# Kernel optimization log

Measured on AMD Instinct MI355X. Metric: run time of the kernel, lower is better.

The kernel has to match this reference:

```python
import jax, jax.numpy as jnp
import numpy as np

N_NODES = 100000
N_EDGES = 1000000
D_IN = 128
D_H = 128
N_CLS = 16


def setup_inputs() -> dict:
    key = jax.random.key(0)
    ks = jax.random.split(key, 12)
    s_in = 1.0 / np.sqrt(D_IN)
    s_h = 1.0 / np.sqrt(D_H)
    s_2h = 1.0 / np.sqrt(2 * D_H)
    return {
        "x": jax.random.normal(ks[0], (N_NODES, D_IN), jnp.float32),
        "edge_index": jax.random.randint(ks[1], (2, N_EDGES), 0, N_NODES, jnp.int64),
        "W_l0": jax.random.normal(ks[2], (D_H, D_IN), jnp.float32) * s_in,
        "b_l0": jnp.zeros((D_H,), jnp.float32),
        "W_r0": jax.random.normal(ks[3], (D_H, D_IN), jnp.float32) * s_in,
        "W_l1": jax.random.normal(ks[4], (D_H, D_H), jnp.float32) * s_h,
        "b_l1": jnp.zeros((D_H,), jnp.float32),
        "W_r1": jax.random.normal(ks[5], (D_H, D_H), jnp.float32) * s_h,
        "W_c": jax.random.normal(ks[6], (D_H, 2 * D_H), jnp.float32) * s_2h,
        "b_c": jnp.zeros((D_H,), jnp.float32),
        "W_o": jax.random.normal(ks[7], (N_CLS, 2 * D_H), jnp.float32) * s_2h,
        "b_o": jnp.zeros((N_CLS,), jnp.float32),
    }


def _sage_conv(x, src, dst, W_l, b_l, W_r, num_nodes):
    # PyG SAGEConv (mean aggr): lin_l(mean of source-neighbor feats) + lin_r(x)
    msgs = x[src]  # [E, d] gather
    agg = jax.ops.segment_sum(msgs, dst, num_segments=num_nodes)
    cnt = jax.ops.segment_sum(jnp.ones((src.shape[0],), x.dtype), dst, num_segments=num_nodes)
    mean = agg / jnp.maximum(cnt, 1.0)[:, None]
    return mean @ W_l.T + b_l + x @ W_r.T


def reference(x, edge_index, W_l0, b_l0, W_r0, W_l1, b_l1, W_r1, W_c, b_c, W_o, b_o):
    src, dst = edge_index[0], edge_index[1]
    n = x.shape[0]
    for W_l, b_l, W_r in ((W_l0, b_l0, W_r0), (W_l1, b_l1, W_r1)):
        x_old = x
        h = jax.nn.relu(_sage_conv(x, src, dst, W_l, b_l, W_r, n))
        x = jnp.concatenate([x_old, h], axis=-1)  # [N, 2*hidden]
        x = jax.nn.relu(x @ W_c.T + b_c)
        # dropout: identity (eval mode)
    edge_feats = jnp.concatenate([x[src], x[dst]], axis=-1)  # [E, 2*hidden]
    return edge_feats @ W_o.T + b_o
```

## Files before the change

kernel.cpp:

```cpp
#include <hip/hip_runtime.h>
#include <hip/hip_bf16.h>

#define NN 100000
#define NE 1000000
#define D  128
#define NC 16

typedef short short8 __attribute__((ext_vector_type(8)));
typedef float f32x4  __attribute__((ext_vector_type(4)));

__device__ __forceinline__ float bf2f(ushort u) {
  union { unsigned int i; float f; } v; v.i = ((unsigned int)u) << 16; return v.f;
}
__device__ __forceinline__ ushort f2bf(float f) {
  union { float f; unsigned int i; } v; v.f = f;
  unsigned int x = v.i;
  return (ushort)((x + 0x7FFFu + ((x >> 16) & 1u)) >> 16);
}

__global__ void sniff_k(const ushort* __restrict__ xr, const unsigned int* __restrict__ ei,
                        int* __restrict__ flags) {
  if (threadIdx.x != 0 || blockIdx.x != 0) return;
  int f32 = 0;
  for (int i = 0; i < 128; ++i) {
    unsigned int e = ((unsigned int)xr[i] >> 7) & 0xFFu;
    if (e < 97u || e > 157u) f32 = 1;
  }
  flags[0] = f32;
  unsigned int s = 0;
  for (int i = 1; i < 256; i += 2) s |= ei[i];
  flags[1] = (s == 0) ? 1 : 0;
}

__global__ void convert_idx_k(const int* __restrict__ ei, const int* __restrict__ flags,
                              int* __restrict__ idx, int n) {
  int i = blockIdx.x * blockDim.x + threadIdx.x;
  if (i >= n) return;
  int v = flags[1] ? ei[2 * i] : ei[i];
  v = v < 0 ? 0 : (v >= NN ? NN - 1 : v);
  idx[i] = v;
}

__global__ void convert_x_k(const void* __restrict__ xin, const int* __restrict__ flags,
                            ushort* __restrict__ xb) {
  int i = blockIdx.x * blockDim.x + threadIdx.x;
  const int n4 = NN * D / 4;
  if (i >= n4) return;
  ushort4 o;
  if (flags[0]) {
    float4 v = ((const float4*)xin)[i];
    o.x = f2bf(v.x); o.y = f2bf(v.y); o.z = f2bf(v.z); o.w = f2bf(v.w);
  } else {
    o = ((const ushort4*)xin)[i];
  }
  ((ushort4*)xb)[i] = o;
}

struct WPtrs { const void* p[10]; };
#define WTOT 102800
__global__ void convert_w_k(WPtrs w, const int* __restrict__ flags, ushort* __restrict__ wb) {
  const int off[10] = {0, 16384, 32768, 49152, 65536, 98304, 102400, 102528, 102656, 102784};
  int i = blockIdx.x * blockDim.x + threadIdx.x;
  if (i >= WTOT) return;
  int seg = 0;
  #pragma unroll
  for (int s2 = 1; s2 < 10; ++s2) if (i >= off[s2]) seg = s2;
  int j = i - off[seg];
  wb[i] = flags[0] ? f2bf(((const float*)w.p[seg])[j]) : ((const ushort*)w.p[seg])[j];
}

#define BSH 9
#define NBKT ((NN + 511) >> BSH)
#define MS_NBLK 256
#define MS_EPB ((NE + MS_NBLK - 1) / MS_NBLK)
#define CSR_CAP 8192

__global__ __launch_bounds__(256) void hist_k(const int* __restrict__ dst,
                                              int* __restrict__ bhist) {
  __shared__ int h[NBKT];
  for (int t = threadIdx.x; t < NBKT; t += 256) h[t] = 0;
  __syncthreads();
  const int stride = gridDim.x * blockDim.x;
  for (int i = blockIdx.x * blockDim.x + threadIdx.x; i < NE; i += stride)
    atomicAdd(&h[dst[i] >> BSH], 1);
  __syncthreads();
  for (int t = threadIdx.x; t < NBKT; t += 256) if (h[t]) atomicAdd(&bhist[t], h[t]);
}

__global__ __launch_bounds__(256) void scanb_k(const int* __restrict__ bhist,
                                               int* __restrict__ bstart,
                                               int* __restrict__ bcur) {
  __shared__ int tmp[256];
  const int t = threadIdx.x;
  int v = (t < NBKT) ? bhist[t] : 0;
  tmp[t] = v;
  __syncthreads();
  for (int s = 1; s < 256; s <<= 1) {
    int u = (t >= s) ? tmp[t - s] : 0;
    __syncthreads();
    tmp[t] += u;
    __syncthreads();
  }
  if (t < NBKT) {
    int ex = tmp[t] - v;
    bstart[t] = ex;
    bcur[t] = ex;
  }
  if (t == NBKT - 1) bstart[NBKT] = tmp[t];
}

__global__ __launch_bounds__(512) void msplit_k(const int* __restrict__ src,
                                                const int* __restrict__ dst,
                                                int* __restrict__ bcur,
                                                int2* __restrict__ ebuf) {
  __shared__ int2 ep[MS_EPB];
  __shared__ int hist[NBKT];
  __shared__ int gbase[NBKT];
  const int e0 = blockIdx.x * MS_EPB;
  int n = NE - e0; if (n > MS_EPB) n = MS_EPB;
  for (int t = threadIdx.x; t < NBKT; t += 512) hist[t] = 0;
  __syncthreads();
  for (int t = threadIdx.x; t < n; t += 512) {
    int s = src[e0 + t], d = dst[e0 + t];
    ep[t] = make_int2(s, d);
    atomicAdd(&hist[d >> BSH], 1);
  }
  __syncthreads();
  for (int t = threadIdx.x; t < NBKT; t += 512) {
    gbase[t] = atomicAdd(&bcur[t], hist[t]);
    hist[t] = 0;
  }
  __syncthreads();
  for (int t = threadIdx.x; t < n; t += 512) {
    int2 p = ep[t];
    int b = p.y >> BSH;
    int loc = atomicAdd(&hist[b], 1);
    ebuf[gbase[b] + loc] = p;
  }
}

__global__ __launch_bounds__(512) void csr_k(const int2* __restrict__ ebuf,
                                             const int* __restrict__ bstart,
                                             int* __restrict__ off,
                                             int* __restrict__ nbr) {
  __shared__ int cnt_s[512];
  __shared__ int ofs_s[512];
  __shared__ int lnbr[CSR_CAP];
  const int b = blockIdx.x;
  const int n0 = b << BSH;
  int nn = NN - n0; if (nn > 512) nn = 512;
  const int e0 = bstart[b], e1 = bstart[b + 1];
  const int n = e1 - e0;
  const int t = threadIdx.x;
  cnt_s[t] = 0;
  __syncthreads();
  for (int i = t; i < n; i += 512)
    atomicAdd(&cnt_s[ebuf[e0 + i].y - n0], 1);
  __syncthreads();
  int v = cnt_s[t];
  ofs_s[t] = v;
  __syncthreads();
  for (int s = 1; s < 512; s <<= 1) {
    int u = (t >= s) ? ofs_s[t - s] : 0;
    __syncthreads();
    ofs_s[t] += u;
    __syncthreads();
  }
  const int excl = ofs_s[t] - v;
  if (t < nn) off[n0 + t] = e0 + excl;
  if (b == gridDim.x - 1 && t == 0) off[NN] = e1;
  cnt_s[t] = excl;
  __syncthreads();
  if (n <= CSR_CAP) {
    for (int i = t; i < n; i += 512) {
      int2 p = ebuf[e0 + i];
      int loc = atomicAdd(&cnt_s[p.y - n0], 1);
      lnbr[loc] = p.x;
    }
    __syncthreads();
    for (int i = t; i < n; i += 512) nbr[e0 + i] = lnbr[i];
  } else {
    for (int i = t; i < n; i += 512) {
      int2 p = ebuf[e0 + i];
      int loc = atomicAdd(&cnt_s[p.y - n0], 1);
      nbr[e0 + loc] = p.x;
    }
  }
}

__global__ __launch_bounds__(256) void agg_k(
    const ushort* __restrict__ X, const int* __restrict__ nbr,
    const int* __restrict__ off, ushort* __restrict__ mean) {
  const int wave = threadIdx.x >> 6, lane = threadIdx.x & 63;
  const int node = blockIdx.x * 4 + wave;
  if (node >= NN) return;
  const int j0 = off[node], j1 = off[node + 1];
  const int g = lane >> 4, l15 = lane & 15;
  float a[8];
  #pragma unroll
  for (int k = 0; k < 8; ++k) a[k] = 0.f;
  int j = j0 + g;
  for (; j + 4 < j1; j += 8) {
    int s0 = nbr[j], s1 = nbr[j + 4];
    uint4 v0 = *(const uint4*)(X + (size_t)s0 * D + l15 * 8);
    uint4 v1 = *(const uint4*)(X + (size_t)s1 * D + l15 * 8);
    unsigned int w0[4] = {v0.x, v0.y, v0.z, v0.w};
    unsigned int w1[4] = {v1.x, v1.y, v1.z, v1.w};
    #pragma unroll
    for (int k = 0; k < 4; ++k) {
      union { unsigned int u; float f; } lo0, hi0, lo1, hi1;
      lo0.u = w0[k] << 16; hi0.u = w0[k] & 0xffff0000u;
      lo1.u = w1[k] << 16; hi1.u = w1[k] & 0xffff0000u;
      a[2 * k]     += lo0.f + lo1.f;
      a[2 * k + 1] += hi0.f + hi1.f;
    }
  }
  if (j < j1) {
    uint4 v0 = *(const uint4*)(X + (size_t)nbr[j] * D + l15 * 8);
    unsigned int w0[4] = {v0.x, v0.y, v0.z, v0.w};
    #pragma unroll
    for (int k = 0; k < 4; ++k) {
      union { unsigned int u; float f; } lo0, hi0;
      lo0.u = w0[k] << 16; hi0.u = w0[k] & 0xffff0000u;
      a[2 * k]     += lo0.f;
      a[2 * k + 1] += hi0.f;
    }
  }
  #pragma unroll
  for (int k = 0; k < 8; ++k) {
    a[k] += __shfl_xor(a[k], 16, 64);
    a[k] += __shfl_xor(a[k], 32, 64);
  }
  if (g == 0) {
    int deg = j1 - j0;
    float inv = 1.f / (float)(deg > 1 ? deg : 1);
    uint4 o;
    o.x = (unsigned int)f2bf(a[0] * inv) | ((unsigned int)f2bf(a[1] * inv) << 16);
    o.y = (unsigned int)f2bf(a[2] * inv) | ((unsigned int)f2bf(a[3] * inv) << 16);
    o.z = (unsigned int)f2bf(a[4] * inv) | ((unsigned int)f2bf(a[5] * inv) << 16);
    o.w = (unsigned int)f2bf(a[6] * inv) | ((unsigned int)f2bf(a[7] * inv) << 16);
    *(uint4*)(mean + (size_t)node * D + l15 * 8) = o;
  }
}

__global__ __launch_bounds__(256) void gemm_dual(
    const ushort* __restrict__ A1, const ushort* __restrict__ A2,
    const ushort* __restrict__ W1, const ushort* __restrict__ W2, int ldw,
    const ushort* __restrict__ bias, ushort* __restrict__ Y, int nrows)
{
  __shared__ ushort wlds[32 * 64 * 8];
  const int tid = threadIdx.x;
  const int wave = tid >> 6, lane = tid & 63;
  const int l15 = lane & 15, q = lane >> 4;
  const int m0 = blockIdx.x * 128 + wave * 32;

  f32x4 acc[2][8];
  #pragma unroll
  for (int rt = 0; rt < 2; ++rt)
    #pragma unroll
    for (int c = 0; c < 8; ++c) acc[rt][c] = (f32x4){0.f, 0.f, 0.f, 0.f};

  for (int phase = 0; phase < 2; ++phase) {
    const ushort* W = phase ? W2 : W1;
    const ushort* A = phase ? A2 : A1;
    __syncthreads();
    #pragma unroll
    for (int it = 0; it < 8; ++it) {
      int combo = it * 4 + wave;
      int c = combo >> 2, ks = combo & 3;
      *(uint4*)(&wlds[(combo * 64 + lane) * 8]) =
          *(const uint4*)(W + (size_t)(c * 16 + l15) * ldw + ks * 32 + q * 8);
    }
    __syncthreads();
    #pragma unroll
    for (int ks = 0; ks < 4; ++ks) {
      short8 af[2];
      #pragma unroll
      for (int rt = 0; rt < 2; ++rt) {
        int row = m0 + rt * 16 + l15;
        if (row > nrows - 1) row = nrows - 1;
        af[rt] = *(const short8*)(A + (size_t)row * D + ks * 32 + q * 8);
      }
      #pragma unroll
      for (int c = 0; c < 8; ++c) {
        short8 bf = *(const short8*)(&wlds[((c * 4 + ks) * 64 + lane) * 8]);
        acc[0][c] = __builtin_amdgcn_mfma_f32_16x16x32_bf16(af[0], bf, acc[0][c], 0, 0, 0);
        acc[1][c] = __builtin_amdgcn_mfma_f32_16x16x32_bf16(af[1], bf, acc[1][c], 0, 0, 0);
      }
    }
  }
  #pragma unroll
  for (int c = 0; c < 8; ++c) {
    float b = bf2f(bias[c * 16 + l15]);
    #pragma unroll
    for (int rt = 0; rt < 2; ++rt) {
      #pragma unroll
      for (int r = 0; r < 4; ++r) {
        int row = m0 + rt * 16 + q * 4 + r;
        if (row < nrows) {
          float v = acc[rt][c][r] + b;
          v = v > 0.f ? v : 0.f;
          Y[(size_t)row * D + c * 16 + l15] = f2bf(v);
        }
      }
    }
  }
}

__global__ __launch_bounds__(256) void gemm_po(
    const ushort* __restrict__ X2, const ushort* __restrict__ Wo, float* __restrict__ P)
{
  __shared__ ushort wlds[8 * 64 * 8];
  const int tid = threadIdx.x, wave = tid >> 6, lane = tid & 63;
  const int l15 = lane & 15, q = lane >> 4;
  const int m0 = blockIdx.x * 64 + wave * 16;
  #pragma unroll
  for (int it = 0; it < 2; ++it) {
    int combo = it * 4 + wave;
    int c = combo >> 2, ks = combo & 3;
    *(uint4*)(&wlds[(combo * 64 + lane) * 8]) =
        *(const uint4*)(Wo + (size_t)l15 * 256 + c * 128 + ks * 32 + q * 8);
  }
  __syncthreads();
  f32x4 acc[2] = {(f32x4){0.f,0.f,0.f,0.f}, (f32x4){0.f,0.f,0.f,0.f}};
  #pragma unroll
  for (int ks = 0; ks < 4; ++ks) {
    int row = m0 + l15; if (row > NN - 1) row = NN - 1;
    short8 af = *(const short8*)(X2 + (size_t)row * D + ks * 32 + q * 8);
    #pragma unroll
    for (int c = 0; c < 2; ++c) {
      short8 bf = *(const short8*)(&wlds[((c * 4 + ks) * 64 + lane) * 8]);
      acc[c] = __builtin_amdgcn_mfma_f32_16x16x32_bf16(af, bf, acc[c], 0, 0, 0);
    }
  }
  #pragma unroll
  for (int c = 0; c < 2; ++c)
    #pragma unroll
    for (int r = 0; r < 4; ++r) {
      int row = m0 + q * 4 + r;
      if (row < NN) P[(size_t)row * 32 + c * 16 + l15] = acc[c][r];
    }
}

__global__ __launch_bounds__(256) void edge_sum_k(
    const float* __restrict__ P, const int* __restrict__ src, const int* __restrict__ dst,
    const ushort* __restrict__ bo, const int* __restrict__ flags,
    void* __restrict__ outv, int E)
{
  int gid = blockIdx.x * blockDim.x + threadIdx.x;
  if (gid >= E * 4) return;
  int e = gid >> 2, cq = (gid & 3) * 4;
  int s = src[e], d = dst[e];
  float4 a = *(const float4*)(P + (size_t)s * 32 + cq);
  float4 b = *(const float4*)(P + (size_t)d * 32 + 16 + cq);
  float4 o;
  o.x = a.x + b.x + bf2f(bo[cq + 0]);
  o.y = a.y + b.y + bf2f(bo[cq + 1]);
  o.z = a.z + b.z + bf2f(bo[cq + 2]);
  o.w = a.w + b.w + bf2f(bo[cq + 3]);
  if (flags[0]) {
    ((float4*)outv)[gid] = o;
  } else {
    ushort4 u;
    u.x = f2bf(o.x); u.y = f2bf(o.y); u.z = f2bf(o.z); u.w = f2bf(o.w);
    ((ushort4*)outv)[gid] = u;
  }
}

extern "C" void kernel_launch(void* const* d_in, const int* in_sizes, int n_in,
                              void* d_out, int out_size, void* d_ws, size_t ws_size,
                              hipStream_t stream) {
  const void* x_in = d_in[0];
  const int*  ei   = (const int*)d_in[1];

  char* ws = (char*)d_ws;
  int*    idx   = (int*)(ws + 0);
  int*    bhist = (int*)(ws + 8000000);
  int*    flags = (int*)(ws + 8400000);
  ushort* wb    = (ushort*)(ws + 8400256);
  int*    off   = (int*)(ws + 8605856);
  int*    bstart= (int*)(ws + 9005872);
  int*    nbr   = (int*)(ws + 9405872);
  int*    bcur  = (int*)(ws + 13405872);
  ushort* buf1  = (ushort*)(ws + 13407440);
  ushort* buf2  = (ushort*)(ws + 39007440);
  ushort* dscr  = (ushort*)d_out;
  float*  P     = (float*)buf1;
  int2*   ebuf  = (int2*)buf1;

  int* src = idx;
  int* dst = idx + NE;

  ushort* Wl0 = wb + 0,      *Wr0 = wb + 16384, *Wl1 = wb + 32768, *Wr1 = wb + 49152;
  ushort* Wc  = wb + 65536,  *Wo  = wb + 98304;
  ushort* bl0 = wb + 102400, *bl1 = wb + 102528, *bc = wb + 102656, *bo = wb + 102784;

  WPtrs w;
  w.p[0] = d_in[2];  w.p[1] = d_in[4];  w.p[2] = d_in[5];  w.p[3] = d_in[7];
  w.p[4] = d_in[8];  w.p[5] = d_in[10]; w.p[6] = d_in[3];  w.p[7] = d_in[6];
  w.p[8] = d_in[9];  w.p[9] = d_in[11];

  const int gblocks = (NN + 127) / 128;
  const int n4 = NN * D / 4;
  const int agrid = (NN + 3) / 4;

  sniff_k<<<1, 64, 0, stream>>>((const ushort*)x_in, (const unsigned int*)ei, flags);
  convert_idx_k<<<(2 * NE + 255) / 256, 256, 0, stream>>>(ei, flags, idx, 2 * NE);
  convert_x_k<<<(n4 + 255) / 256, 256, 0, stream>>>(x_in, flags, buf2);
  convert_w_k<<<(WTOT + 255) / 256, 256, 0, stream>>>(w, flags, wb);

  (void)hipMemsetAsync(bhist, 0, NBKT * sizeof(int), stream);
  hist_k<<<256, 256, 0, stream>>>(dst, bhist);
  scanb_k<<<1, 256, 0, stream>>>(bhist, bstart, bcur);
  msplit_k<<<MS_NBLK, 512, 0, stream>>>(src, dst, bcur, ebuf);
  csr_k<<<NBKT, 512, 0, stream>>>(ebuf, bstart, off, nbr);

  agg_k<<<agrid, 256, 0, stream>>>(buf2, nbr, off, dscr);
  gemm_dual<<<gblocks, 256, 0, stream>>>(dscr, buf2, Wl0, Wr0, D, bl0, buf1, NN);
  gemm_dual<<<gblocks, 256, 0, stream>>>(buf2, buf1, Wc, Wc + D, 2 * D, bc, dscr, NN);

  agg_k<<<agrid, 256, 0, stream>>>(dscr, nbr, off, buf2);
  gemm_dual<<<gblocks, 256, 0, stream>>>(buf2, dscr, Wl1, Wr1, D, bl1, buf1, NN);
  gemm_dual<<<gblocks, 256, 0, stream>>>(dscr, buf1, Wc, Wc + D, 2 * D, bc, buf2, NN);

  gemm_po<<<(NN + 63) / 64, 256, 0, stream>>>(buf2, Wo, P);
  edge_sum_k<<<(4 * NE + 255) / 256, 256, 0, stream>>>(P, src, dst, bo, flags, d_out, NE);
}
```

Measured before the change: 433.5 us.

## Fuse dst histogram into index conversion and drop LDS weight staging in GEMMs

Folds the bucket histogram over dst into the index-conversion kernel and zeroes the histogram inside the sniff kernel, which removes a memset and a separate histogram launch along with one re-read of dst. The GEMM kernels stop staging weights in shared memory. Each wave now reads its weight fragments straight from global memory (cached, since the weights are small) and preloads all A fragments into registers. gemm_dual also gets a launch-bounds occupancy hint. This removes LDS traffic and block barriers, but every wave now issues its own global weight loads and register pressure goes up.

```diff
diff --git a/kernel.cpp b/kernel.cpp
--- a/kernel.cpp
+++ b/kernel.cpp
@@ -18,9 +18,17 @@
   return (ushort)((x + 0x7FFFu + ((x >> 16) & 1u)) >> 16);
 }
 
+#define BSH 9
+#define NBKT ((NN + 511) >> BSH)
+#define MS_NBLK 256
+#define MS_EPB ((NE + MS_NBLK - 1) / MS_NBLK)
+#define CSR_CAP 8192
+
 __global__ void sniff_k(const ushort* __restrict__ xr, const unsigned int* __restrict__ ei,
-                        int* __restrict__ flags) {
-  if (threadIdx.x != 0 || blockIdx.x != 0) return;
+                        int* __restrict__ flags, int* __restrict__ bhist) {
+  int t = threadIdx.x;
+  if (t < NBKT) bhist[t] = 0;
+  if (t != 0 || blockIdx.x != 0) return;
   int f32 = 0;
   for (int i = 0; i < 128; ++i) {
     unsigned int e = ((unsigned int)xr[i] >> 7) & 0xFFu;
@@ -32,13 +40,21 @@
   flags[1] = (s == 0) ? 1 : 0;
 }
 
-__global__ void convert_idx_k(const int* __restrict__ ei, const int* __restrict__ flags,
-                              int* __restrict__ idx, int n) {
-  int i = blockIdx.x * blockDim.x + threadIdx.x;
-  if (i >= n) return;
-  int v = flags[1] ? ei[2 * i] : ei[i];
-  v = v < 0 ? 0 : (v >= NN ? NN - 1 : v);
-  idx[i] = v;
+__global__ __launch_bounds__(256) void convert_idx_k(
+    const int* __restrict__ ei, const int* __restrict__ flags,
+    int* __restrict__ idx, int* __restrict__ bhist) {
+  __shared__ int h[NBKT];
+  const int i = blockIdx.x * 256 + threadIdx.x;
+  for (int t = threadIdx.x; t < NBKT; t += 256) h[t] = 0;
+  __syncthreads();
+  if (i < 2 * NE) {
+    int v = flags[1] ? ei[2 * i] : ei[i];
+    v = v < 0 ? 0 : (v >= NN ? NN - 1 : v);
+    idx[i] = v;
+    if (i >= NE) atomicAdd(&h[v >> BSH], 1);
+  }
+  __syncthreads();
+  for (int t = threadIdx.x; t < NBKT; t += 256) if (h[t]) atomicAdd(&bhist[t], h[t]);
 }
 
 __global__ void convert_x_k(const void* __restrict__ xin, const int* __restrict__ flags,
@@ -67,24 +83,6 @@
   for (int s2 = 1; s2 < 10; ++s2) if (i >= off[s2]) seg = s2;
   int j = i - off[seg];
   wb[i] = flags[0] ? f2bf(((const float*)w.p[seg])[j]) : ((const ushort*)w.p[seg])[j];
-}
-
-#define BSH 9
-#define NBKT ((NN + 511) >> BSH)
-#define MS_NBLK 256
-#define MS_EPB ((NE + MS_NBLK - 1) / MS_NBLK)
-#define CSR_CAP 8192
-
-__global__ __launch_bounds__(256) void hist_k(const int* __restrict__ dst,
-                                              int* __restrict__ bhist) {
-  __shared__ int h[NBKT];
-  for (int t = threadIdx.x; t < NBKT; t += 256) h[t] = 0;
-  __syncthreads();
-  const int stride = gridDim.x * blockDim.x;
-  for (int i = blockIdx.x * blockDim.x + threadIdx.x; i < NE; i += stride)
-    atomicAdd(&h[dst[i] >> BSH], 1);
-  __syncthreads();
-  for (int t = threadIdx.x; t < NBKT; t += 256) if (h[t]) atomicAdd(&bhist[t], h[t]);
 }
 
 __global__ __launch_bounds__(256) void scanb_k(const int* __restrict__ bhist,
@@ -243,12 +241,11 @@
   }
 }
 
-__global__ __launch_bounds__(256) void gemm_dual(
+__global__ __launch_bounds__(256, 3) void gemm_dual(
     const ushort* __restrict__ A1, const ushort* __restrict__ A2,
     const ushort* __restrict__ W1, const ushort* __restrict__ W2, int ldw,
     const ushort* __restrict__ bias, ushort* __restrict__ Y, int nrows)
 {
-  __shared__ ushort wlds[32 * 64 * 8];
   const int tid = threadIdx.x;
   const int wave = tid >> 6, lane = tid & 63;
   const int l15 = lane & 15, q = lane >> 4;
@@ -260,32 +257,27 @@
     #pragma unroll
     for (int c = 0; c < 8; ++c) acc[rt][c] = (f32x4){0.f, 0.f, 0.f, 0.f};
 
+  int r0 = m0 + l15;      if (r0 > nrows - 1) r0 = nrows - 1;
+  int r1 = m0 + 16 + l15; if (r1 > nrows - 1) r1 = nrows - 1;
+
+  #pragma unroll
   for (int phase = 0; phase < 2; ++phase) {
     const ushort* W = phase ? W2 : W1;
     const ushort* A = phase ? A2 : A1;
-    __syncthreads();
-    #pragma unroll
-    for (int it = 0; it < 8; ++it) {
-      int combo = it * 4 + wave;
-      int c = combo >> 2, ks = combo & 3;
-      *(uint4*)(&wlds[(combo * 64 + lane) * 8]) =
-          *(const uint4*)(W + (size_t)(c * 16 + l15) * ldw + ks * 32 + q * 8);
-    }
-    __syncthreads();
+    short8 af0[4], af1[4];
     #pragma unroll
     for (int ks = 0; ks < 4; ++ks) {
-      short8 af[2];
+      af0[ks] = *(const short8*)(A + (size_t)r0 * D + ks * 32 + q * 8);
+      af1[ks] = *(const short8*)(A + (size_t)r1 * D + ks * 32 + q * 8);
+    }
+    #pragma unroll 2
+    for (int c = 0; c < 8; ++c) {
+      const ushort* wc = W + (size_t)(c * 16 + l15) * ldw + q * 8;
       #pragma unroll
-      for (int rt = 0; rt < 2; ++rt) {
-        int row = m0 + rt * 16 + l15;
-        if (row > nrows - 1) row = nrows - 1;
-        af[rt] = *(const short8*)(A + (size_t)row * D + ks * 32 + q * 8);
-      }
-      #pragma unroll
-      for (int c = 0; c < 8; ++c) {
-        short8 bf = *(const short8*)(&wlds[((c * 4 + ks) * 64 + lane) * 8]);
-        acc[0][c] = __builtin_amdgcn_mfma_f32_16x16x32_bf16(af[0], bf, acc[0][c], 0, 0, 0);
-        acc[1][c] = __builtin_amdgcn_mfma_f32_16x16x32_bf16(af[1], bf, acc[1][c], 0, 0, 0);
+      for (int ks = 0; ks < 4; ++ks) {
+        short8 bf = *(const short8*)(wc + ks * 32);
+        acc[0][c] = __builtin_amdgcn_mfma_f32_16x16x32_bf16(af0[ks], bf, acc[0][c], 0, 0, 0);
+        acc[1][c] = __builtin_amdgcn_mfma_f32_16x16x32_bf16(af1[ks], bf, acc[1][c], 0, 0, 0);
       }
     }
   }
@@ -310,26 +302,17 @@
 __global__ __launch_bounds__(256) void gemm_po(
     const ushort* __restrict__ X2, const ushort* __restrict__ Wo, float* __restrict__ P)
 {
-  __shared__ ushort wlds[8 * 64 * 8];
   const int tid = threadIdx.x, wave = tid >> 6, lane = tid & 63;
   const int l15 = lane & 15, q = lane >> 4;
   const int m0 = blockIdx.x * 64 + wave * 16;
-  #pragma unroll
-  for (int it = 0; it < 2; ++it) {
-    int combo = it * 4 + wave;
-    int c = combo >> 2, ks = combo & 3;
-    *(uint4*)(&wlds[(combo * 64 + lane) * 8]) =
-        *(const uint4*)(Wo + (size_t)l15 * 256 + c * 128 + ks * 32 + q * 8);
-  }
-  __syncthreads();
+  int row = m0 + l15; if (row > NN - 1) row = NN - 1;
   f32x4 acc[2] = {(f32x4){0.f,0.f,0.f,0.f}, (f32x4){0.f,0.f,0.f,0.f}};
   #pragma unroll
   for (int ks = 0; ks < 4; ++ks) {
-    int row = m0 + l15; if (row > NN - 1) row = NN - 1;
     short8 af = *(const short8*)(X2 + (size_t)row * D + ks * 32 + q * 8);
     #pragma unroll
     for (int c = 0; c < 2; ++c) {
-      short8 bf = *(const short8*)(&wlds[((c * 4 + ks) * 64 + lane) * 8]);
+      short8 bf = *(const short8*)(Wo + (size_t)l15 * 256 + c * 128 + ks * 32 + q * 8);
       acc[c] = __builtin_amdgcn_mfma_f32_16x16x32_bf16(af, bf, acc[c], 0, 0, 0);
     }
   }
@@ -337,8 +320,8 @@
   for (int c = 0; c < 2; ++c)
     #pragma unroll
     for (int r = 0; r < 4; ++r) {
-      int row = m0 + q * 4 + r;
-      if (row < NN) P[(size_t)row * 32 + c * 16 + l15] = acc[c][r];
+      int orow = m0 + q * 4 + r;
+      if (orow < NN) P[(size_t)orow * 32 + c * 16 + l15] = acc[c][r];
     }
 }
 
@@ -404,13 +387,11 @@
   const int n4 = NN * D / 4;
   const int agrid = (NN + 3) / 4;
 
-  sniff_k<<<1, 64, 0, stream>>>((const ushort*)x_in, (const unsigned int*)ei, flags);
-  convert_idx_k<<<(2 * NE + 255) / 256, 256, 0, stream>>>(ei, flags, idx, 2 * NE);
+  sniff_k<<<1, 256, 0, stream>>>((const ushort*)x_in, (const unsigned int*)ei, flags, bhist);
+  convert_idx_k<<<(2 * NE + 255) / 256, 256, 0, stream>>>(ei, flags, idx, bhist);
   convert_x_k<<<(n4 + 255) / 256, 256, 0, stream>>>(x_in, flags, buf2);
   convert_w_k<<<(WTOT + 255) / 256, 256, 0, stream>>>(w, flags, wb);
 
-  (void)hipMemsetAsync(bhist, 0, NBKT * sizeof(int), stream);
-  hist_k<<<256, 256, 0, stream>>>(dst, bhist);
   scanb_k<<<1, 256, 0, stream>>>(bhist, bstart, bcur);
   msplit_k<<<MS_NBLK, 512, 0, stream>>>(src, dst, bcur, ebuf);
   csr_k<<<NBKT, 512, 0, stream>>>(ebuf, bstart, off, nbr);
```

New measurement: 797.7 us. 84.0% more time.
